# Performance work log

Measured on AMD Instinct MI355X. Metric: run time of the kernel, lower is better.

Reference implementation:

```python
import jax, jax.numpy as jnp
import numpy as np

N1 = 200000          # total nodes in batched data1
B = 8                # graphs in data1 (equal-sized)
NPG = N1 // B        # nodes per graph = 25000
N2 = 199             # total nodes in data2 (forced by fc1 in_features 9950 = 50*199)
K = 50               # SortAggregation k
E1 = 2000000
E2 = 3184
F_IN = 128
LN_EPS = 1e-5


def _lin(x, W, b):
    return x @ W + b


def _gin(x, ei, W1a, b1a, W1b, b1b, W2a, b2a, W2b, b2b):
    # GINConv with eps=0: nn((1+eps)*x + sum_{j in N(i)} x_j); messages flow ei[0] -> ei[1]
    agg = jnp.zeros_like(x).at[ei[1]].add(x[ei[0]])
    h = _lin(jax.nn.relu(_lin(x + agg, W1a, b1a)), W1b, b1b)
    h = jax.nn.relu(h)
    agg = jnp.zeros_like(h).at[ei[1]].add(h[ei[0]])
    h2 = _lin(jax.nn.relu(_lin(h + agg, W2a, b2a)), W2b, b2b)
    return jax.nn.relu(h2)


def _cdist(a, b):
    # torch.cdist p=2: [N1, D] x [N2, D] -> [N1, N2]
    sq = (a * a).sum(-1, keepdims=True) + (b * b).sum(-1)[None, :] - 2.0 * (a @ b.T)
    return jnp.sqrt(jnp.maximum(sq, 0.0))


def _sort_pool(x_dense, k):
    # DGCNN sort pooling: sort nodes per graph by last channel, descending; take top-k
    # x_dense: [B, N, D] (all graphs full, so no fill-value padding needed)
    order = jnp.argsort(-x_dense[:, :, -1], axis=-1)[:, :k]       # [B, k]
    return jnp.take_along_axis(x_dense, order[:, :, None], axis=1)  # [B, k, D]


def _layernorm(x, g, b):
    mu = x.mean(-1, keepdims=True)
    var = ((x - mu) ** 2).mean(-1, keepdims=True)
    return (x - mu) * jax.lax.rsqrt(var + LN_EPS) * g + b


def setup_inputs() -> dict:
    key = jax.random.key(0)
    ks = jax.random.split(key, 32)
    s = 0.05
    inp = {
        "x1": jax.random.normal(ks[0], (N1, F_IN), jnp.float32),
        "edge_index1": jax.random.randint(ks[1], (2, E1), 0, N1, jnp.int64),
        "batch1": jnp.repeat(jnp.arange(B, dtype=jnp.int64), NPG),
        "x2": jax.random.normal(ks[2], (N2, F_IN), jnp.float32),
        "edge_index2": jax.random.randint(ks[3], (2, E2), 0, N2, jnp.int64),
        # GIN conv1 MLP: Linear(128,128), ReLU, Linear(128,128)
        "W1a": jax.random.normal(ks[4], (F_IN, 128), jnp.float32) * s,
        "b1a": jnp.zeros((128,), jnp.float32),
        "W1b": jax.random.normal(ks[5], (128, 128), jnp.float32) * s,
        "b1b": jnp.zeros((128,), jnp.float32),
        # GIN conv2 MLP: Linear(128,64), ReLU, Linear(64,64)
        "W2a": jax.random.normal(ks[6], (128, 64), jnp.float32) * s,
        "b2a": jnp.zeros((64,), jnp.float32),
        "W2b": jax.random.normal(ks[7], (64, 64), jnp.float32) * s,
        "b2b": jnp.zeros((64,), jnp.float32),
        # head
        "fc1_W": jax.random.normal(ks[8], (K * N2, 128), jnp.float32) * 0.01,
        "fc1_b": jnp.zeros((128,), jnp.float32),
        "g1": jnp.ones((128,), jnp.float32),
        "be1": jnp.zeros((128,), jnp.float32),
        "fc2_W": jax.random.normal(ks[9], (128, 64), jnp.float32) * s,
        "fc2_b": jnp.zeros((64,), jnp.float32),
        "g2": jnp.ones((64,), jnp.float32),
        "be2": jnp.zeros((64,), jnp.float32),
        "fc3_W": jax.random.normal(ks[10], (64, 1), jnp.float32) * s,
        "fc3_b": jnp.zeros((1,), jnp.float32),
    }
    return inp


def reference(x1, edge_index1, batch1, x2, edge_index2,
              W1a, b1a, W1b, b1b, W2a, b2a, W2b, b2b,
              fc1_W, fc1_b, g1, be1, fc2_W, fc2_b, g2, be2, fc3_W, fc3_b):
    out1 = _gin(x1, edge_index1, W1a, b1a, W1b, b1b, W2a, b2a, W2b, b2b)  # [N1, 64]
    out2 = _gin(x2, edge_index2, W1a, b1a, W1b, b1b, W2a, b2a, W2b, b2b)  # [N2, 64]
    d = _cdist(out1, out2)                       # [N1, N2]
    # graphs in data1 are equal-sized (batch1 = repeat(arange(B), NPG)) -> dense batch is a reshape
    dense = d.reshape(B, NPG, N2)
    pooled = _sort_pool(dense, K).reshape(B, K * N2)  # [B, 9950]
    h = jax.nn.relu(_layernorm(_lin(pooled, fc1_W, fc1_b), g1, be1))
    h = jax.nn.relu(_layernorm(_lin(h, fc2_W, fc2_b), g2, be2))
    return jax.nn.sigmoid(_lin(h, fc3_W, fc3_b))  # [B, 1]
```

## Files before the change

kernel.cpp:

```cpp
#include <hip/hip_runtime.h>
#include <math.h>


#define CPB 64
#define FKS 64

__global__ __launch_bounds__(256) void hist_kernel(const int* __restrict__ dst, int E,
                                                   int* __restrict__ counts) {
    int e = blockIdx.x * 256 + threadIdx.x;
    if (e < E) atomicAdd(&counts[dst[e]], 1);
}

__global__ __launch_bounds__(256) void chunksum_kernel(const int* __restrict__ in, int total,
                                                       int* __restrict__ bsum) {
    __shared__ int red[256];
    int t = threadIdx.x;
    int base = blockIdx.x * 1024 + t * 4;
    int s = 0;
#pragma unroll
    for (int j = 0; j < 4; ++j) { int i = base + j; if (i < total) s += in[i]; }
    red[t] = s; __syncthreads();
    for (int off = 128; off; off >>= 1) { if (t < off) red[t] += red[t + off]; __syncthreads(); }
    if (t == 0) bsum[blockIdx.x] = red[0];
}

__global__ __launch_bounds__(256) void scanchunk_kernel(const int* __restrict__ in, int total,
                                                        const int* __restrict__ baseArr,
                                                        int* __restrict__ out,
                                                        int* __restrict__ out2) {
    __shared__ int tsum[256];
    int t = threadIdx.x;
    int base_i = blockIdx.x * 1024 + t * 4;
    int v[4];
#pragma unroll
    for (int j = 0; j < 4; ++j) v[j] = (base_i + j < total) ? in[base_i + j] : 0;
    int l0 = 0, l1 = v[0], l2 = v[0] + v[1], l3 = l2 + v[2];
    int s = l3 + v[3];
    tsum[t] = s; __syncthreads();
    for (int off = 1; off < 256; off <<= 1) {
        int x = (t >= off) ? tsum[t - off] : 0;
        __syncthreads();
        tsum[t] += x;
        __syncthreads();
    }
    int cb = baseArr ? baseArr[blockIdx.x] : 0;
    int te = cb + tsum[t] - s;
    int outs[4] = { te + l0, te + l1, te + l2, te + l3 };
#pragma unroll
    for (int j = 0; j < 4; ++j) {
        int i = base_i + j;
        if (i < total) { out[i] = outs[j]; if (out2) out2[i] = outs[j]; }
    }
}

__global__ __launch_bounds__(256) void fill_kernel(const int* __restrict__ src,
                                                   const int* __restrict__ dst, int E,
                                                   int* __restrict__ cur, int* __restrict__ csr) {
    int e = blockIdx.x * 256 + threadIdx.x;
    if (e < E) {
        int d = dst[e];
        int p = atomicAdd(&cur[d], 1);
        csr[p] = src[e];
    }
}

template <int KI, int KO, bool BIAS, bool RELU>
__global__ __launch_bounds__(256) void gemm_kernel(const float* __restrict__ X,
                                                   const float* __restrict__ Wm,
                                                   const float* __restrict__ bias,
                                                   float* __restrict__ Y, int N) {
    constexpr int TPR = KO / 4;
    constexpr int RPT = KO / 16;
    constexpr int XS = 68;
    __shared__ __align__(16) float wl[32 * KO];
    __shared__ __align__(16) float xt[32 * XS];
    const int t = threadIdx.x;
    const int r0 = blockIdx.x * 64;
    const int tx = t % TPR, ty = t / TPR;
    float4 acc[RPT];
#pragma unroll
    for (int r = 0; r < RPT; ++r) acc[r] = make_float4(0.f, 0.f, 0.f, 0.f);

    for (int kb = 0; kb < KI; kb += 32) {
        __syncthreads();
#pragma unroll
        for (int i = t; i < 32 * KO / 4; i += 256)
            ((float4*)wl)[i] = ((const float4*)Wm)[kb * KO / 4 + i];
#pragma unroll
        for (int L = t; L < 512; L += 256) {
            int row = L >> 3, kq = L & 7;
            int gr = r0 + row;
            float4 v = make_float4(0.f, 0.f, 0.f, 0.f);
            if (gr < N) v = *(const float4*)(X + (size_t)gr * KI + kb + kq * 4);
            xt[(kq * 4 + 0) * XS + row] = v.x;
            xt[(kq * 4 + 1) * XS + row] = v.y;
            xt[(kq * 4 + 2) * XS + row] = v.z;
            xt[(kq * 4 + 3) * XS + row] = v.w;
        }
        __syncthreads();
#pragma unroll
        for (int k = 0; k < 32; ++k) {
            float4 wv = ((const float4*)wl)[k * TPR + tx];
            const float4* xp = (const float4*)(xt + k * XS + ty * RPT);
#pragma unroll
            for (int rq = 0; rq < RPT / 4; ++rq) {
                float4 xv = xp[rq];
                acc[rq*4+0].x += xv.x * wv.x; acc[rq*4+0].y += xv.x * wv.y;
                acc[rq*4+0].z += xv.x * wv.z; acc[rq*4+0].w += xv.x * wv.w;
                acc[rq*4+1].x += xv.y * wv.x; acc[rq*4+1].y += xv.y * wv.y;
                acc[rq*4+1].z += xv.y * wv.z; acc[rq*4+1].w += xv.y * wv.w;
                acc[rq*4+2].x += xv.z * wv.x; acc[rq*4+2].y += xv.z * wv.y;
                acc[rq*4+2].z += xv.z * wv.z; acc[rq*4+2].w += xv.z * wv.w;
                acc[rq*4+3].x += xv.w * wv.x; acc[rq*4+3].y += xv.w * wv.y;
                acc[rq*4+3].z += xv.w * wv.z; acc[rq*4+3].w += xv.w * wv.w;
            }
        }
    }
    float4 b4 = make_float4(0.f, 0.f, 0.f, 0.f);
    if (BIAS) b4 = ((const float4*)bias)[tx];
#pragma unroll
    for (int r = 0; r < RPT; ++r) {
        int gr = r0 + ty * RPT + r;
        if (gr < N) {
            float4 o = make_float4(acc[r].x + b4.x, acc[r].y + b4.y,
                                   acc[r].z + b4.z, acc[r].w + b4.w);
            if (RELU) {
                o.x = fmaxf(o.x, 0.f); o.y = fmaxf(o.y, 0.f);
                o.z = fmaxf(o.z, 0.f); o.w = fmaxf(o.w, 0.f);
            }
            *(float4*)(Y + (size_t)gr * KO + tx * 4) = o;
        }
    }
}

template <int VEC>
__global__ __launch_bounds__(256) void agg_kernel(const float* __restrict__ x,
                                                  const int* __restrict__ rs,
                                                  const int* __restrict__ csr,
                                                  const float* __restrict__ bias,
                                                  float* __restrict__ out, int N) {
    const int NPB = 256 / VEC;
    const int t = threadIdx.x;
    const int node = blockIdx.x * NPB + t / VEC;
    const int c = t % VEC;
    if (node >= N) return;
    const int W = VEC * 4;
    float4 acc = ((const float4*)(x + (size_t)node * W))[c];
    const int s1 = rs[node + 1];
    for (int k = rs[node]; k < s1; ++k) {
        int src = csr[k];
        float4 v = ((const float4*)(x + (size_t)src * W))[c];
        acc.x += v.x; acc.y += v.y; acc.z += v.z; acc.w += v.w;
    }
    float4 b4 = ((const float4*)bias)[c];
    acc.x = fmaxf(acc.x + b4.x, 0.f);
    acc.y = fmaxf(acc.y + b4.y, 0.f);
    acc.z = fmaxf(acc.z + b4.z, 0.f);
    acc.w = fmaxf(acc.w + b4.w, 0.f);
    ((float4*)(out + (size_t)node * W))[c] = acc;
}

__global__ __launch_bounds__(256) void scores_kernel(const float* __restrict__ out1,
                                                     const float* __restrict__ out2,
                                                     double* __restrict__ sc, int N) {
    const int t = threadIdx.x;
    const int node = blockIdx.x * 4 + (t >> 6);
    const int lane = t & 63;
    if (node >= N) return;
    float a = out1[(size_t)node * 64 + lane];
    float bv = out2[198 * 64 + lane];
    double na = (double)a * a;
    double nb = (double)bv * bv;
    double dd = (double)a * bv;
    for (int off = 32; off; off >>= 1) {
        na += __shfl_xor(na, off);
        nb += __shfl_xor(nb, off);
        dd += __shfl_xor(dd, off);
    }
    if (lane == 0) {
        double sq = na + nb - 2.0 * dd;
        sc[node] = (sq > 0.0) ? sqrt(sq) : 0.0;
    }
}

__global__ __launch_bounds__(256) void topkA_kernel(const double* __restrict__ sc,
                                                    double* __restrict__ cv,
                                                    int* __restrict__ ci, int npg) {
    const int g = blockIdx.x / CPB, cb = blockIdx.x % CPB;
    const int chunk = (npg + CPB - 1) / CPB;
    const int base = cb * chunk;
    const int len = (npg - base < chunk) ? (npg - base) : chunk;
    const int t = threadIdx.x;
    __shared__ double lv[400];
    __shared__ double wvs[4];
    __shared__ int wss[4];
    const double* s = sc + (size_t)g * npg;
    for (int i = t; i < chunk; i += 256)
        lv[i] = (i < len) ? s[base + i] : -1.0e300;
    __syncthreads();
    const int ob = (g * CPB + cb) * 50;
    for (int r = 0; r < 50; ++r) {
        double bv = -1.0e300; int bs = 0x3fffffff;
        for (int i = t; i < chunk; i += 256) {
            double v = lv[i];
            if (v > bv || (v == bv && i < bs)) { bv = v; bs = i; }
        }
#pragma unroll
        for (int off = 32; off; off >>= 1) {
            double ov = __shfl_xor(bv, off);
            int os = __shfl_xor(bs, off);
            if (ov > bv || (ov == bv && os < bs)) { bv = ov; bs = os; }
        }
        if ((t & 63) == 0) { wvs[t >> 6] = bv; wss[t >> 6] = bs; }
        __syncthreads();
        if (t == 0) {
#pragma unroll
            for (int w = 1; w < 4; ++w)
                if (wvs[w] > bv || (wvs[w] == bv && wss[w] < bs)) { bv = wvs[w]; bs = wss[w]; }
            cv[ob + r] = bv;
            ci[ob + r] = base + bs;
            lv[bs] = -1.0e300;
        }
        __syncthreads();
    }
}

__global__ __launch_bounds__(256) void topkB_kernel(const double* __restrict__ cv,
                                                    const int* __restrict__ ci,
                                                    int* __restrict__ topk) {
    const int g = blockIdx.x, t = threadIdx.x;
    const int M = CPB * 50;
    __shared__ double lv[CPB * 50];
    __shared__ int li[CPB * 50];
    __shared__ double wvs[4];
    __shared__ int wis[4], wss[4];
    for (int i = t; i < M; i += 256) {
        lv[i] = cv[(size_t)g * M + i];
        li[i] = ci[(size_t)g * M + i];
    }
    __syncthreads();
    for (int r = 0; r < 50; ++r) {
        double bv = -1.0e300; int bi = 0x3fffffff, bs = 0;
        for (int i = t; i < M; i += 256) {
            double v = lv[i]; int idx = li[i];
            if (v > bv || (v == bv && idx < bi)) { bv = v; bi = idx; bs = i; }
        }
#pragma unroll
        for (int off = 32; off; off >>= 1) {
            double ov = __shfl_xor(bv, off);
            int oi = __shfl_xor(bi, off);
            int os = __shfl_xor(bs, off);
            if (ov > bv || (ov == bv && oi < bi)) { bv = ov; bi = oi; bs = os; }
        }
        if ((t & 63) == 0) { wvs[t >> 6] = bv; wis[t >> 6] = bi; wss[t >> 6] = bs; }
        __syncthreads();
        if (t == 0) {
#pragma unroll
            for (int w = 1; w < 4; ++w)
                if (wvs[w] > bv || (wvs[w] == bv && wis[w] < bi)) {
                    bv = wvs[w]; bi = wis[w]; bs = wss[w];
                }
            topk[g * 50 + r] = bi;
            lv[bs] = -1.0e300;
        }
        __syncthreads();
    }
}

__global__ __launch_bounds__(256) void pooled_kernel(const float* __restrict__ out1,
                                                     const float* __restrict__ out2,
                                                     const int* __restrict__ topk,
                                                     float* __restrict__ pooled, int npg) {
    const int bk = blockIdx.x;
    const int g = bk / 50, kk = bk % 50;
    __shared__ float arow[64];
    const int t = threadIdx.x;
    const int node = g * npg + topk[g * 50 + kk];
    if (t < 64) arow[t] = out1[(size_t)node * 64 + t];
    __syncthreads();
    if (t < 199) {
        double na = 0.0, nb = 0.0, dd = 0.0;
        for (int k2 = 0; k2 < 64; ++k2) {
            double a = arow[k2];
            double b = out2[t * 64 + k2];
            na += a * a; nb += b * b; dd += a * b;
        }
        double sq = na + nb - 2.0 * dd;
        pooled[(size_t)g * 9950 + kk * 199 + t] = (float)((sq > 0.0) ? sqrt(sq) : 0.0);
    }
}

__global__ __launch_bounds__(256) void fc1_partial_kernel(const float* __restrict__ pooled,
                                                          const float* __restrict__ W,
                                                          double* __restrict__ part) {
    const int b = blockIdx.x >> 6;
    const int ks = blockIdx.x & (FKS - 1);
    const int t = threadIdx.x;
    const int f = t & 127, half = t >> 7;
    const int C = (9950 + FKS - 1) / FKS;
    const int i0 = ks * C;
    const int i1 = (i0 + C < 9950) ? (i0 + C) : 9950;
    const float* p = pooled + (size_t)b * 9950;
    double acc = 0.0;
    for (int i = i0 + half; i < i1; i += 2)
        acc += (double)p[i] * (double)W[(size_t)i * 128 + f];
    __shared__ double red[256];
    red[t] = acc; __syncthreads();
    if (half == 0)
        part[((size_t)b * FKS + ks) * 128 + f] = red[f] + red[128 + f];
}

__global__ __launch_bounds__(128) void fc1_reduce_kernel(const double* __restrict__ part,
                                                         const float* __restrict__ bias,
                                                         float* __restrict__ z1) {
    const int b = blockIdx.x, f = threadIdx.x;
    double acc = 0.0;
    for (int ks = 0; ks < FKS; ++ks)
        acc += part[((size_t)b * FKS + ks) * 128 + f];
    z1[b * 128 + f] = (float)(acc + (double)bias[f]);
}

__global__ __launch_bounds__(128) void head_kernel(const float* __restrict__ z1,
                                                   const float* __restrict__ g1,
                                                   const float* __restrict__ be1,
                                                   const float* __restrict__ W2,
                                                   const float* __restrict__ b2,
                                                   const float* __restrict__ g2,
                                                   const float* __restrict__ be2,
                                                   const float* __restrict__ W3,
                                                   const float* __restrict__ b3,
                                                   float* __restrict__ out) {
    const int b = blockIdx.x, t = threadIdx.x;
    __shared__ double red[128];
    __shared__ float shy[128];
    __shared__ float sh2[64];
    float z = z1[b * 128 + t];
    red[t] = z; __syncthreads();
    for (int off = 64; off; off >>= 1) { if (t < off) red[t] += red[t + off]; __syncthreads(); }
    double mu = red[0] / 128.0; __syncthreads();
    double dv = (double)z - mu;
    red[t] = dv * dv; __syncthreads();
    for (int off = 64; off; off >>= 1) { if (t < off) red[t] += red[t + off]; __syncthreads(); }
    double var = red[0] / 128.0; __syncthreads();
    float y = (float)(dv / sqrt(var + 1e-5)) * g1[t] + be1[t];
    shy[t] = fmaxf(y, 0.f); __syncthreads();
    double a2 = 0.0;
    if (t < 64) {
        for (int i = 0; i < 128; ++i) a2 += (double)shy[i] * (double)W2[i * 64 + t];
        a2 += (double)b2[t];
    }
    red[t] = (t < 64) ? a2 : 0.0; __syncthreads();
    for (int off = 64; off; off >>= 1) { if (t < off) red[t] += red[t + off]; __syncthreads(); }
    double mu2 = red[0] / 64.0; __syncthreads();
    double dv2 = a2 - mu2;
    red[t] = (t < 64) ? dv2 * dv2 : 0.0; __syncthreads();
    for (int off = 64; off; off >>= 1) { if (t < off) red[t] += red[t + off]; __syncthreads(); }
    double var2 = red[0] / 64.0; __syncthreads();
    if (t < 64) {
        float h2 = (float)(dv2 / sqrt(var2 + 1e-5)) * g2[t] + be2[t];
        sh2[t] = fmaxf(h2, 0.f);
    }
    __syncthreads();
    red[t] = (t < 64) ? (double)sh2[t] * (double)W3[t] : 0.0; __syncthreads();
    for (int off = 64; off; off >>= 1) { if (t < off) red[t] += red[t + off]; __syncthreads(); }
    if (t == 0) {
        double zf = red[0] + (double)b3[0];
        out[b] = (float)(1.0 / (1.0 + exp(-zf)));
    }
}

extern "C" void kernel_launch(void* const* d_in, const int* in_sizes, int n_in,
                              void* d_out, int out_size, void* d_ws, size_t ws_size,
                              hipStream_t stream) {
    (void)n_in; (void)out_size; (void)ws_size;
    const float* x1  = (const float*)d_in[0];
    const int*   ei1 = (const int*)d_in[1];
    const float* x2  = (const float*)d_in[3];
    const int*   ei2 = (const int*)d_in[4];
    const float* W1a = (const float*)d_in[5];
    const float* b1a = (const float*)d_in[6];
    const float* W1b = (const float*)d_in[7];
    const float* b1b = (const float*)d_in[8];
    const float* W2a = (const float*)d_in[9];
    const float* b2a = (const float*)d_in[10];
    const float* W2b = (const float*)d_in[11];
    const float* b2b = (const float*)d_in[12];
    const float* f1W = (const float*)d_in[13];
    const float* f1b = (const float*)d_in[14];
    const float* g1  = (const float*)d_in[15];
    const float* be1 = (const float*)d_in[16];
    const float* f2W = (const float*)d_in[17];
    const float* f2b = (const float*)d_in[18];
    const float* g2  = (const float*)d_in[19];
    const float* be2 = (const float*)d_in[20];
    const float* f3W = (const float*)d_in[21];
    const float* f3b = (const float*)d_in[22];
    float* out = (float*)d_out;

    const int n1 = in_sizes[0] / 128;
    const int e1 = in_sizes[1] / 2;
    const int n2 = in_sizes[3] / 128;
    const int e2 = in_sizes[4] / 2;
    const int npg = n1 / 8;

    char* p = (char*)d_ws;
    auto alloc = [&](size_t bytes) { char* r = p; p += (bytes + 255) & ~(size_t)255; return r; };
    float*  A    = (float*)alloc((size_t)n1 * 128 * 4);
    float*  Bb   = (float*)alloc((size_t)n1 * 128 * 4);
    double* sc   = (double*)alloc((size_t)n1 * 8);
    int*    rs1  = (int*)alloc((size_t)(n1 + 1) * 4);
    int*    cur1 = (int*)alloc((size_t)(n1 + 1) * 4);
    int*    csr1 = (int*)alloc((size_t)e1 * 4);
    int*    bsum = (int*)alloc(4096);
    int*    rs2  = (int*)alloc((size_t)(n2 + 1) * 4);
    int*    cur2 = (int*)alloc((size_t)(n2 + 1) * 4);
    int*    csr2 = (int*)alloc((size_t)e2 * 4);
    float*  G2A  = (float*)alloc((size_t)n2 * 128 * 4);
    float*  G2B  = (float*)alloc((size_t)n2 * 128 * 4);
    float*  o2   = (float*)alloc((size_t)n2 * 64 * 4);
    double* cndv = (double*)alloc((size_t)8 * CPB * 50 * 8);
    int*    cndi = (int*)alloc((size_t)8 * CPB * 50 * 4);
    int*    tk   = (int*)alloc(8 * 50 * 4);
    float*  pld  = (float*)alloc((size_t)8 * 9950 * 4);
    double* f1p  = (double*)alloc((size_t)8 * FKS * 128 * 8);
    float*  z1   = (float*)alloc(8 * 128 * 4);

    const int* src1 = ei1;           const int* dst1 = ei1 + e1;
    const int* src2 = ei2;           const int* dst2 = ei2 + e2;

    hipMemsetAsync(rs1, 0, (size_t)(n1 + 1) * 4, stream);
    hipMemsetAsync(rs2, 0, (size_t)(n2 + 1) * 4, stream);
    hist_kernel<<<(e1 + 255) / 256, 256, 0, stream>>>(dst1, e1, rs1);
    hist_kernel<<<(e2 + 255) / 256, 256, 0, stream>>>(dst2, e2, rs2);
    int tot1 = n1 + 1, nch1 = (tot1 + 1023) / 1024;
    chunksum_kernel<<<nch1, 256, 0, stream>>>(rs1, tot1, bsum);
    scanchunk_kernel<<<1, 256, 0, stream>>>(bsum, nch1, nullptr, bsum, nullptr);
    scanchunk_kernel<<<nch1, 256, 0, stream>>>(rs1, tot1, bsum, rs1, cur1);
    fill_kernel<<<(e1 + 255) / 256, 256, 0, stream>>>(src1, dst1, e1, cur1, csr1);
    int tot2 = n2 + 1, nch2 = (tot2 + 1023) / 1024;
    chunksum_kernel<<<nch2, 256, 0, stream>>>(rs2, tot2, bsum);
    scanchunk_kernel<<<1, 256, 0, stream>>>(bsum, nch2, nullptr, bsum, nullptr);
    scanchunk_kernel<<<nch2, 256, 0, stream>>>(rs2, tot2, bsum, rs2, cur2);
    fill_kernel<<<(e2 + 255) / 256, 256, 0, stream>>>(src2, dst2, e2, cur2, csr2);

    int gb1 = (n1 + 63) / 64;
    gemm_kernel<128, 128, false, false><<<gb1, 256, 0, stream>>>(x1, W1a, nullptr, A, n1);
    agg_kernel<32><<<(n1 + 7) / 8, 256, 0, stream>>>(A, rs1, csr1, b1a, Bb, n1);
    gemm_kernel<128, 128, true, true><<<gb1, 256, 0, stream>>>(Bb, W1b, b1b, A, n1);
    gemm_kernel<128, 64, false, false><<<gb1, 256, 0, stream>>>(A, W2a, nullptr, Bb, n1);
    agg_kernel<16><<<(n1 + 15) / 16, 256, 0, stream>>>(Bb, rs1, csr1, b2a, A, n1);
    gemm_kernel<64, 64, true, true><<<gb1, 256, 0, stream>>>(A, W2b, b2b, Bb, n1);

    int gb2 = (n2 + 63) / 64;
    gemm_kernel<128, 128, false, false><<<gb2, 256, 0, stream>>>(x2, W1a, nullptr, G2A, n2);
    agg_kernel<32><<<(n2 + 7) / 8, 256, 0, stream>>>(G2A, rs2, csr2, b1a, G2B, n2);
    gemm_kernel<128, 128, true, true><<<gb2, 256, 0, stream>>>(G2B, W1b, b1b, G2A, n2);
    gemm_kernel<128, 64, false, false><<<gb2, 256, 0, stream>>>(G2A, W2a, nullptr, G2B, n2);
    agg_kernel<16><<<(n2 + 15) / 16, 256, 0, stream>>>(G2B, rs2, csr2, b2a, G2A, n2);
    gemm_kernel<64, 64, true, true><<<gb2, 256, 0, stream>>>(G2A, W2b, b2b, o2, n2);

    scores_kernel<<<(n1 + 3) / 4, 256, 0, stream>>>(Bb, o2, sc, n1);
    topkA_kernel<<<8 * CPB, 256, 0, stream>>>(sc, cndv, cndi, npg);
    topkB_kernel<<<8, 256, 0, stream>>>(cndv, cndi, tk);
    pooled_kernel<<<400, 256, 0, stream>>>(Bb, o2, tk, pld, npg);

    fc1_partial_kernel<<<8 * FKS, 256, 0, stream>>>(pld, f1W, f1p);
    fc1_reduce_kernel<<<8, 128, 0, stream>>>(f1p, f1b, z1);
    head_kernel<<<8, 128, 0, stream>>>(z1, g1, be1, f2W, f2b, g2, be2, f3W, f3b, out);
}
```

Baseline: 1.310 ms.

## Fuse consecutive GIN MLP GEMMs and unroll neighbor aggregation loop

Adds a fused kernel that computes relu(X@W1b+b1b) into shared memory and multiplies it by W2a in the same block, so the 128-wide intermediate for 200k nodes is never written to or read back from global memory. The aggregation kernel is unrolled by four with two accumulators, which puts more independent gather loads in flight. Buffer roles are swapped so the downstream scores and pooling kernels read from A. The cost is a larger shared-memory footprint per block (about 60KB), which may lower occupancy.

```diff
diff --git a/kernel.cpp b/kernel.cpp
--- a/kernel.cpp
+++ b/kernel.cpp
@@ -133,6 +133,99 @@
     }
 }
 
+__global__ __launch_bounds__(256) void gemm23_kernel(const float* __restrict__ X,
+                                                     const float* __restrict__ W1,
+                                                     const float* __restrict__ b1,
+                                                     const float* __restrict__ W2,
+                                                     float* __restrict__ Y, int N) {
+    __shared__ __align__(16) float wl[32 * 128];
+    __shared__ __align__(16) float xt[32 * 68];
+    __shared__ __align__(16) float ht[128 * 68];
+    const int t = threadIdx.x;
+    const int r0 = blockIdx.x * 64;
+
+    const int tx = t % 32, ty = t / 32;
+    float4 acc[8];
+#pragma unroll
+    for (int r = 0; r < 8; ++r) acc[r] = make_float4(0.f, 0.f, 0.f, 0.f);
+    for (int kb = 0; kb < 128; kb += 32) {
+        __syncthreads();
+#pragma unroll
+        for (int i = t; i < 1024; i += 256)
+            ((float4*)wl)[i] = ((const float4*)W1)[kb * 32 + i];
+#pragma unroll
+        for (int L = t; L < 512; L += 256) {
+            int row = L >> 3, kq = L & 7;
+            int gr = r0 + row;
+            float4 v = make_float4(0.f, 0.f, 0.f, 0.f);
+            if (gr < N) v = *(const float4*)(X + (size_t)gr * 128 + kb + kq * 4);
+            xt[(kq * 4 + 0) * 68 + row] = v.x;
+            xt[(kq * 4 + 1) * 68 + row] = v.y;
+            xt[(kq * 4 + 2) * 68 + row] = v.z;
+            xt[(kq * 4 + 3) * 68 + row] = v.w;
+        }
+        __syncthreads();
+#pragma unroll
+        for (int k = 0; k < 32; ++k) {
+            float4 wv = ((const float4*)wl)[k * 32 + tx];
+            const float4* xp = (const float4*)(xt + k * 68 + ty * 8);
+#pragma unroll
+            for (int rq = 0; rq < 2; ++rq) {
+                float4 xv = xp[rq];
+                acc[rq*4+0].x += xv.x * wv.x; acc[rq*4+0].y += xv.x * wv.y;
+                acc[rq*4+0].z += xv.x * wv.z; acc[rq*4+0].w += xv.x * wv.w;
+                acc[rq*4+1].x += xv.y * wv.x; acc[rq*4+1].y += xv.y * wv.y;
+                acc[rq*4+1].z += xv.y * wv.z; acc[rq*4+1].w += xv.y * wv.w;
+                acc[rq*4+2].x += xv.z * wv.x; acc[rq*4+2].y += xv.z * wv.y;
+                acc[rq*4+2].z += xv.z * wv.z; acc[rq*4+2].w += xv.z * wv.w;
+                acc[rq*4+3].x += xv.w * wv.x; acc[rq*4+3].y += xv.w * wv.y;
+                acc[rq*4+3].z += xv.w * wv.z; acc[rq*4+3].w += xv.w * wv.w;
+            }
+        }
+    }
+    {
+        float4 b4 = ((const float4*)b1)[tx];
+#pragma unroll
+        for (int r = 0; r < 8; ++r) {
+            int row = ty * 8 + r;
+            float4 v = acc[r];
+            ht[(tx * 4 + 0) * 68 + row] = fmaxf(v.x + b4.x, 0.f);
+            ht[(tx * 4 + 1) * 68 + row] = fmaxf(v.y + b4.y, 0.f);
+            ht[(tx * 4 + 2) * 68 + row] = fmaxf(v.z + b4.z, 0.f);
+            ht[(tx * 4 + 3) * 68 + row] = fmaxf(v.w + b4.w, 0.f);
+        }
+    }
+    const int tx2 = t % 16, ty2 = t / 16;
+    float4 acc2[4];
+#pragma unroll
+    for (int r = 0; r < 4; ++r) acc2[r] = make_float4(0.f, 0.f, 0.f, 0.f);
+    for (int kb = 0; kb < 128; kb += 32) {
+        __syncthreads();
+#pragma unroll
+        for (int i = t; i < 512; i += 256)
+            ((float4*)wl)[i] = ((const float4*)W2)[kb * 16 + i];
+        __syncthreads();
+#pragma unroll
+        for (int k = 0; k < 32; ++k) {
+            float4 wv = ((const float4*)wl)[k * 16 + tx2];
+            float4 xv = *(const float4*)(ht + (kb + k) * 68 + ty2 * 4);
+            acc2[0].x += xv.x * wv.x; acc2[0].y += xv.x * wv.y;
+            acc2[0].z += xv.x * wv.z; acc2[0].w += xv.x * wv.w;
+            acc2[1].x += xv.y * wv.x; acc2[1].y += xv.y * wv.y;
+            acc2[1].z += xv.y * wv.z; acc2[1].w += xv.y * wv.w;
+            acc2[2].x += xv.z * wv.x; acc2[2].y += xv.z * wv.y;
+            acc2[2].z += xv.z * wv.z; acc2[2].w += xv.z * wv.w;
+            acc2[3].x += xv.w * wv.x; acc2[3].y += xv.w * wv.y;
+            acc2[3].z += xv.w * wv.z; acc2[3].w += xv.w * wv.w;
+        }
+    }
+#pragma unroll
+    for (int r = 0; r < 4; ++r) {
+        int gr = r0 + ty2 * 4 + r;
+        if (gr < N) *(float4*)(Y + (size_t)gr * 64 + tx2 * 4) = acc2[r];
+    }
+}
+
 template <int VEC>
 __global__ __launch_bounds__(256) void agg_kernel(const float* __restrict__ x,
                                                   const int* __restrict__ rs,
@@ -144,20 +237,34 @@
     const int node = blockIdx.x * NPB + t / VEC;
     const int c = t % VEC;
     if (node >= N) return;
-    const int W = VEC * 4;
-    float4 acc = ((const float4*)(x + (size_t)node * W))[c];
+    const float4* xb = (const float4*)x;
+    float4 a0 = xb[(size_t)node * VEC + c];
+    float4 a1 = make_float4(0.f, 0.f, 0.f, 0.f);
+    int k = rs[node];
     const int s1 = rs[node + 1];
-    for (int k = rs[node]; k < s1; ++k) {
-        int src = csr[k];
-        float4 v = ((const float4*)(x + (size_t)src * W))[c];
-        acc.x += v.x; acc.y += v.y; acc.z += v.z; acc.w += v.w;
+    for (; k + 4 <= s1; k += 4) {
+        int i0 = csr[k], i1 = csr[k + 1], i2 = csr[k + 2], i3 = csr[k + 3];
+        float4 v0 = xb[(size_t)i0 * VEC + c];
+        float4 v1 = xb[(size_t)i1 * VEC + c];
+        float4 v2 = xb[(size_t)i2 * VEC + c];
+        float4 v3 = xb[(size_t)i3 * VEC + c];
+        a0.x += v0.x; a0.y += v0.y; a0.z += v0.z; a0.w += v0.w;
+        a1.x += v1.x; a1.y += v1.y; a1.z += v1.z; a1.w += v1.w;
+        a0.x += v2.x; a0.y += v2.y; a0.z += v2.z; a0.w += v2.w;
+        a1.x += v3.x; a1.y += v3.y; a1.z += v3.z; a1.w += v3.w;
+    }
+    for (; k < s1; ++k) {
+        int i = csr[k];
+        float4 v = xb[(size_t)i * VEC + c];
+        a0.x += v.x; a0.y += v.y; a0.z += v.z; a0.w += v.w;
     }
     float4 b4 = ((const float4*)bias)[c];
-    acc.x = fmaxf(acc.x + b4.x, 0.f);
-    acc.y = fmaxf(acc.y + b4.y, 0.f);
-    acc.z = fmaxf(acc.z + b4.z, 0.f);
-    acc.w = fmaxf(acc.w + b4.w, 0.f);
-    ((float4*)(out + (size_t)node * W))[c] = acc;
+    float4 o;
+    o.x = fmaxf(a0.x + a1.x + b4.x, 0.f);
+    o.y = fmaxf(a0.y + a1.y + b4.y, 0.f);
+    o.z = fmaxf(a0.z + a1.z + b4.z, 0.f);
+    o.w = fmaxf(a0.w + a1.w + b4.w, 0.f);
+    ((float4*)out)[(size_t)node * VEC + c] = o;
 }
 
 __global__ __launch_bounds__(256) void scores_kernel(const float* __restrict__ out1,
@@ -446,23 +553,21 @@
     int gb1 = (n1 + 63) / 64;
     gemm_kernel<128, 128, false, false><<<gb1, 256, 0, stream>>>(x1, W1a, nullptr, A, n1);
     agg_kernel<32><<<(n1 + 7) / 8, 256, 0, stream>>>(A, rs1, csr1, b1a, Bb, n1);
-    gemm_kernel<128, 128, true, true><<<gb1, 256, 0, stream>>>(Bb, W1b, b1b, A, n1);
-    gemm_kernel<128, 64, false, false><<<gb1, 256, 0, stream>>>(A, W2a, nullptr, Bb, n1);
-    agg_kernel<16><<<(n1 + 15) / 16, 256, 0, stream>>>(Bb, rs1, csr1, b2a, A, n1);
-    gemm_kernel<64, 64, true, true><<<gb1, 256, 0, stream>>>(A, W2b, b2b, Bb, n1);
+    gemm23_kernel<<<gb1, 256, 0, stream>>>(Bb, W1b, b1b, W2a, A, n1);
+    agg_kernel<16><<<(n1 + 15) / 16, 256, 0, stream>>>(A, rs1, csr1, b2a, Bb, n1);
+    gemm_kernel<64, 64, true, true><<<gb1, 256, 0, stream>>>(Bb, W2b, b2b, A, n1);
 
     int gb2 = (n2 + 63) / 64;
     gemm_kernel<128, 128, false, false><<<gb2, 256, 0, stream>>>(x2, W1a, nullptr, G2A, n2);
     agg_kernel<32><<<(n2 + 7) / 8, 256, 0, stream>>>(G2A, rs2, csr2, b1a, G2B, n2);
-    gemm_kernel<128, 128, true, true><<<gb2, 256, 0, stream>>>(G2B, W1b, b1b, G2A, n2);
-    gemm_kernel<128, 64, false, false><<<gb2, 256, 0, stream>>>(G2A, W2a, nullptr, G2B, n2);
-    agg_kernel<16><<<(n2 + 15) / 16, 256, 0, stream>>>(G2B, rs2, csr2, b2a, G2A, n2);
-    gemm_kernel<64, 64, true, true><<<gb2, 256, 0, stream>>>(G2A, W2b, b2b, o2, n2);
-
-    scores_kernel<<<(n1 + 3) / 4, 256, 0, stream>>>(Bb, o2, sc, n1);
+    gemm23_kernel<<<gb2, 256, 0, stream>>>(G2B, W1b, b1b, W2a, G2A, n2);
+    agg_kernel<16><<<(n2 + 15) / 16, 256, 0, stream>>>(G2A, rs2, csr2, b2a, G2B, n2);
+    gemm_kernel<64, 64, true, true><<<gb2, 256, 0, stream>>>(G2B, W2b, b2b, o2, n2);
+
+    scores_kernel<<<(n1 + 3) / 4, 256, 0, stream>>>(A, o2, sc, n1);
     topkA_kernel<<<8 * CPB, 256, 0, stream>>>(sc, cndv, cndi, npg);
     topkB_kernel<<<8, 256, 0, stream>>>(cndv, cndi, tk);
-    pooled_kernel<<<400, 256, 0, stream>>>(Bb, o2, tk, pld, npg);
+    pooled_kernel<<<400, 256, 0, stream>>>(A, o2, tk, pld, npg);
 
     fc1_partial_kernel<<<8 * FKS, 256, 0, stream>>>(pld, f1W, f1p);
     fc1_reduce_kernel<<<8, 128, 0, stream>>>(f1p, f1b, z1);
```

Result: no change. 1.324 ms (+1.0%).
